# Kernel tuning notes

Measured on AMD Instinct MI355X. Metric: run time of the kernel, lower is better.

The kernel has to match this reference:

```python
import jax, jax.numpy as jnp
import numpy as np

VOXEL = 64          # voxel_size
MAX_DEPTH = 10.0    # depth_range[1]
SMIN, SMAX = -2.0, 2.0  # spatial_range


def setup_inputs() -> dict:
    key = jax.random.key(0)
    B, H, W = 32, 512, 512
    rgbd = jax.random.uniform(key, (B, 4, H, W), dtype=jnp.float32)
    # scale depth channel to a realistic metric range [0, 8) so that a
    # meaningful fraction of back-projected points falls inside [-2, 2]
    rgbd = rgbd.at[:, 3].multiply(8.0)
    return {"rgbd": rgbd}


def reference(rgbd):
    B, C, H, W = rgbd.shape
    V = VOXEL
    dt = rgbd.dtype

    rgb = jnp.transpose(rgbd[:, :3], (0, 2, 3, 1))   # [B,H,W,3]
    d = rgbd[:, 3]                                   # [B,H,W]

    # intrinsics is None -> default pinhole
    fx = fy = min(H, W) / 2.0
    cx, cy = W / 2.0, H / 2.0

    u = jnp.arange(W, dtype=dt)[None, None, :]       # column index (x)
    v = jnp.arange(H, dtype=dt)[None, :, None]       # row index (y)

    # depth -> pointcloud (per pixel)
    x = (u - cx) * d / fx
    y = (v - cy) * d / fy
    pts = jnp.stack([x, y, d], axis=-1)              # [B,H,W,3]

    depth_valid = (d > 0) & (d < MAX_DEPTH) & jnp.isfinite(d)

    # pointcloud -> voxel coordinates
    coords = jnp.round((pts - SMIN) / (SMAX - SMIN) * (V - 1)).astype(jnp.int32)
    in_range = jnp.all((coords >= 0) & (coords < V), axis=-1)
    mask = depth_valid & in_range                    # [B,H,W]
    coords = jnp.clip(coords, 0, V - 1)

    b_idx = jnp.arange(B, dtype=jnp.int32)[:, None, None]
    lin = ((b_idx * V + coords[..., 0]) * V + coords[..., 1]) * V + coords[..., 2]
    lin = lin.reshape(-1)                            # [B*H*W]
    w = mask.astype(dt).reshape(-1)                  # [B*H*W]

    nseg = B * V * V * V
    count = jax.ops.segment_sum(w, lin, num_segments=nseg)                 # [B*V^3]
    csum = jax.ops.segment_sum(rgb.reshape(-1, 3) * w[:, None], lin,
                               num_segments=nseg)                          # [B*V^3,3]

    occ = (count > 0).astype(dt)                                           # occupancy = 1 where any point lands
    color = jnp.where(count[:, None] > 0,
                      csum / jnp.maximum(count, 1.0)[:, None],
                      jnp.zeros((), dt))                                   # mean color per occupied voxel

    occ = occ.reshape(B, V, V, V)
    color = color.reshape(B, V, V, V, 3).transpose(0, 4, 1, 2, 3)
    return jnp.concatenate([occ[:, None], color], axis=1)  # [B,4,V,V,V]
```

## Files before the change

kernel.cpp:

```cpp
#include <hip/hip_runtime.h>
#include <math.h>


constexpr int V = 64;
constexpr int V3 = V * V * V;
constexpr int Wd = 512, Hd = 512;
constexpr int NPIX = Wd * Hd;
constexpr int NBUCKET = 32 * 64;
constexpr unsigned CAP = 30000;
constexpr float CQ = 32768.0f;
constexpr int PPB = 2048;
constexpr int CHUNKS = NPIX / PPB;

__device__ __forceinline__ bool unproject(int w, int h, float d,
                                          int& ix, int& iy, int& iz) {
    if (!(d > 0.0f) || !(d < 10.0f) || !isfinite(d)) return false;
    const float fx = 256.0f, cx = 256.0f, cy = 256.0f;
    float x = (((float)w - cx) * d) / fx;
    float y = (((float)h - cy) * d) / fx;
    float tx = rintf(((x + 2.0f) * 0.25f) * 63.0f);
    float ty = rintf(((y + 2.0f) * 0.25f) * 63.0f);
    float tz = rintf(((d + 2.0f) * 0.25f) * 63.0f);
    ix = (int)tx; iy = (int)ty; iz = (int)tz;
    return !(ix < 0 || ix >= V || iy < 0 || iy >= V ||
             iz < 0 || iz >= V);
}

__global__ void dtv_cursor_init(unsigned* __restrict__ cursor) {
    int i = blockIdx.x * blockDim.x + threadIdx.x;
    cursor[i] = (unsigned)i * CAP;
}

__global__ void __launch_bounds__(256)
dtv_append4(const float* __restrict__ rgbd,
            unsigned* __restrict__ cursor,
            unsigned long long* __restrict__ entries) {
    int blk = blockIdx.x;
    int b = blk >> 7, chunk = blk & (CHUNKS - 1), t = threadIdx.x;

    __shared__ unsigned lcnt[64];
    __shared__ unsigned lpre[64];
    __shared__ unsigned labs[64];
    __shared__ unsigned long long stage[PPB];
    __shared__ unsigned short bkt[PPB];

    if (t < 64) lcnt[t] = 0;
    __syncthreads();

    const float* bb = rgbd + (size_t)b * 4 * NPIX;
    const float4* r4 = (const float4*)(bb) + chunk * (PPB / 4);
    const float4* g4 = (const float4*)(bb + (size_t)NPIX) + chunk * (PPB / 4);
    const float4* b4 = (const float4*)(bb + (size_t)2 * NPIX) + chunk * (PPB / 4);
    const float4* d4 = (const float4*)(bb + (size_t)3 * NPIX) + chunk * (PPB / 4);
    int pbase = chunk * PPB;

    float4 dv[2], rv[2], gv[2], bv[2];
#pragma unroll
    for (int i = 0; i < 2; ++i) dv[i] = d4[t + i * 256];
#pragma unroll
    for (int i = 0; i < 2; ++i) {
        rv[i] = r4[t + i * 256];
        gv[i] = g4[t + i * 256];
        bv[i] = b4[t + i * 256];
    }

    unsigned meta[8];
#pragma unroll
    for (int i = 0; i < 2; ++i) {
        int p0 = pbase + 4 * (t + i * 256);
#pragma unroll
        for (int j = 0; j < 4; ++j) {
            float d = (j == 0) ? dv[i].x : (j == 1) ? dv[i].y
                    : (j == 2) ? dv[i].z : dv[i].w;
            int pix = p0 + j;
            int h = pix >> 9, w = pix & (Wd - 1);
            int ix, iy, iz;
            if (unproject(w, h, d, ix, iy, iz)) {
                unsigned off = atomicAdd(&lcnt[ix], 1u);
                meta[i * 4 + j] = ((unsigned)ix << 24) | ((unsigned)iy << 18) |
                                  ((unsigned)iz << 12) | off;
            } else {
                meta[i * 4 + j] = 0xFFFFFFFFu;
            }
        }
    }
    __syncthreads();

    if (t < 64) {
        unsigned c = lcnt[t];
        unsigned s = c;
#pragma unroll
        for (int off = 1; off < 64; off <<= 1) {
            unsigned v = __shfl_up(s, off, 64);
            if (t >= off) s += v;
        }
        lpre[t] = s - c;
        labs[t] = c ? atomicAdd(&cursor[b * 64 + t], c) : 0u;
    }
    __syncthreads();

#pragma unroll
    for (int i = 0; i < 2; ++i) {
#pragma unroll
        for (int j = 0; j < 4; ++j) {
            unsigned m = meta[i * 4 + j];
            if (m == 0xFFFFFFFFu) continue;
            unsigned ix = m >> 24, iy = (m >> 18) & 63u, iz = (m >> 12) & 63u;
            unsigned off = m & 0xFFFu;
            float r  = (j == 0) ? rv[i].x : (j == 1) ? rv[i].y
                     : (j == 2) ? rv[i].z : rv[i].w;
            float g  = (j == 0) ? gv[i].x : (j == 1) ? gv[i].y
                     : (j == 2) ? gv[i].z : gv[i].w;
            float bl = (j == 0) ? bv[i].x : (j == 1) ? bv[i].y
                     : (j == 2) ? bv[i].z : bv[i].w;
            unsigned long long r16 = (unsigned long long)(unsigned)rintf(r  * CQ);
            unsigned long long g16 = (unsigned long long)(unsigned)rintf(g  * CQ);
            unsigned long long b16 = (unsigned long long)(unsigned)rintf(bl * CQ);
            unsigned slot = lpre[ix] + off;
            stage[slot] = ((unsigned long long)iy << 54) |
                          ((unsigned long long)iz << 48) |
                          (r16 << 32) | (g16 << 16) | b16;
            bkt[slot] = (unsigned short)ix;
        }
    }
    __syncthreads();

    unsigned total = lpre[63] + lcnt[63];
    for (unsigned e = t; e < total; e += 256) {
        unsigned ix = bkt[e];
        unsigned pos = labs[ix] + (e - lpre[ix]);
        unsigned kk = (unsigned)(b * 64) + ix;
        if (pos < (kk + 1) * CAP)
            entries[(size_t)pos] = stage[e];
    }
}

__global__ void __launch_bounds__(256)
dtv_reduce4(const ulonglong2* __restrict__ entries2,
            const unsigned* __restrict__ cursor,
            float* __restrict__ out) {
    int bq = blockIdx.x;
    int kk = bq >> 2;
    unsigned quad = (unsigned)(bq & 3);
    int b = kk >> 6, ix = kk & 63, t = threadIdx.x;

    __shared__ unsigned long long ldsA[1024];
    __shared__ unsigned long long ldsB[1024];

    unsigned basew = (unsigned)kk * CAP;
    unsigned cnt = cursor[kk] - basew;
    if (cnt > CAP) cnt = CAP;
    unsigned npair = cnt >> 1;
    size_t base2 = (size_t)kk * (CAP / 2);

    ulonglong2 e2;
    if (t < (int)npair) e2 = entries2[base2 + t];

    ulonglong2* zA = (ulonglong2*)ldsA;
    ulonglong2* zB = (ulonglong2*)ldsB;
#pragma unroll
    for (int i = 0; i < 2; ++i) {
        zA[t + i * 256] = ulonglong2{0ULL, 0ULL};
        zB[t + i * 256] = ulonglong2{0ULL, 0ULL};
    }
    __syncthreads();

    auto accum = [&](unsigned long long p) {
        if (((unsigned)(p >> 58) & 3u) != quad) return;
        unsigned iy4 = (unsigned)(p >> 54) & 15u;
        unsigned iz  = (unsigned)(p >> 48) & 63u;
        unsigned v = iy4 * 64u + iz;
        atomicAdd(&ldsA[v], (1ULL << 32) | ((p >> 32) & 0xFFFFULL));
        atomicAdd(&ldsB[v], (((p >> 16) & 0xFFFFULL) << 32) | (p & 0xFFFFULL));
    };

    for (unsigned j = t; j < npair; j += 256) {
        ulonglong2 cur = e2;
        unsigned jn = j + 256;
        if (jn < npair) e2 = entries2[base2 + jn];
        accum(cur.x);
        accum(cur.y);
    }
    if ((cnt & 1u) && t == 0) {
        const unsigned long long* e1 = (const unsigned long long*)entries2;
        accum(e1[(size_t)basew + cnt - 1]);
    }
    __syncthreads();

    float* p0 = out + (size_t)b * 4 * V3 + (size_t)ix * 4096 + quad * 1024;
    int v0 = t * 4;
    float4 o0, o1, o2, o3;
#pragma unroll
    for (int j = 0; j < 4; ++j) {
        unsigned long long A = ldsA[v0 + j], Bw = ldsB[v0 + j];
        unsigned c = (unsigned)(A >> 32);
        float occ = 0.0f, r = 0.0f, g = 0.0f, bl = 0.0f;
        if (c) {
            float inv = 1.0f / (CQ * (float)c);
            occ = 1.0f;
            r  = (float)(unsigned)(A  & 0xFFFFFFFFULL) * inv;
            g  = (float)(unsigned)(Bw >> 32)            * inv;
            bl = (float)(unsigned)(Bw & 0xFFFFFFFFULL)  * inv;
        }
        (&o0.x)[j] = occ; (&o1.x)[j] = r; (&o2.x)[j] = g; (&o3.x)[j] = bl;
    }
    ((float4*)(p0))[t]                  = o0;
    ((float4*)(p0 + (size_t)V3))[t]     = o1;
    ((float4*)(p0 + (size_t)2 * V3))[t] = o2;
    ((float4*)(p0 + (size_t)3 * V3))[t] = o3;
}

__global__ void dtv_scatter_f32(const float* __restrict__ rgbd,
                                float* __restrict__ acc) {
    int idx = blockIdx.x * blockDim.x + threadIdx.x;
    int b   = idx >> 18;
    int pix = idx & (NPIX - 1);
    int h   = pix >> 9;
    int w   = pix & (Wd - 1);
    const float* base = rgbd + (size_t)b * 4 * NPIX;
    float d = base[(size_t)3 * NPIX + pix];
    int ix, iy, iz;
    if (!unproject(w, h, d, ix, iy, iz)) return;
    float r  = base[pix];
    float g  = base[(size_t)NPIX + pix];
    float bl = base[(size_t)2 * NPIX + pix];
    float* ob = acc + (size_t)b * 4 * V3;
    int vlin = (ix * V + iy) * V + iz;
    atomicAdd(ob + vlin, 1.0f);
    atomicAdd(ob + (size_t)V3 + vlin, r);
    atomicAdd(ob + (size_t)2 * V3 + vlin, g);
    atomicAdd(ob + (size_t)3 * V3 + vlin, bl);
}

__global__ void dtv_finalize_f32(float* __restrict__ out) {
    int idx = blockIdx.x * blockDim.x + threadIdx.x;
    int b    = idx >> 18;
    int vlin = idx & (V3 - 1);
    float* p = out + (size_t)b * 4 * V3;
    float c  = p[vlin];
    float r  = p[(size_t)V3 + vlin];
    float g  = p[(size_t)2 * V3 + vlin];
    float bl = p[(size_t)3 * V3 + vlin];
    bool occ = (c > 0.0f);
    p[vlin]                  = occ ? 1.0f : 0.0f;
    p[(size_t)V3 + vlin]     = occ ? (r / c)  : 0.0f;
    p[(size_t)2 * V3 + vlin] = occ ? (g / c)  : 0.0f;
    p[(size_t)3 * V3 + vlin] = occ ? (bl / c) : 0.0f;
}

extern "C" void kernel_launch(void* const* d_in, const int* in_sizes, int n_in,
                              void* d_out, int out_size, void* d_ws, size_t ws_size,
                              hipStream_t stream) {
    const float* rgbd = (const float*)d_in[0];
    float* out = (float*)d_out;
    const int B = in_sizes[0] / (4 * NPIX);

    size_t need = 8192 + (size_t)NBUCKET * CAP * sizeof(unsigned long long);

    if (B == 32 && ws_size >= need) {
        unsigned* cursor = (unsigned*)d_ws;
        unsigned long long* entries =
            (unsigned long long*)((char*)d_ws + 8192);
        dtv_cursor_init<<<NBUCKET / 256, 256, 0, stream>>>(cursor);
        dtv_append4    <<<B * CHUNKS, 256, 0, stream>>>(rgbd, cursor, entries);
        dtv_reduce4    <<<NBUCKET * 4, 256, 0, stream>>>((const ulonglong2*)entries,
                                                         cursor, out);
    } else {
        hipMemsetAsync(d_out, 0, (size_t)out_size * sizeof(float), stream);
        int total_pix = B * NPIX;
        int total_vox = B * V3;
        dtv_scatter_f32 <<<(total_pix + 255) / 256, 256, 0, stream>>>(rgbd, out);
        dtv_finalize_f32<<<(total_vox + 255) / 256, 256, 0, stream>>>(out);
    }
}
```

Measured before the change: 246.5 us.

## Pack bucket index into entry, use nontemporal IO, reorder reduce blocks by load

Color quantization drops to 14 bits so the x-bucket index fits in the 64-bit staged entry, which removes the separate shared-memory bucket array and its writes. Input loads and output stores become nontemporal to avoid cache pollution on streaming data. The reduce grid is remapped so blocks for central x buckets, which likely receive the most points, are scheduled first and the tail is better balanced. Lower color precision increases quantization error in the mean colors.

```diff
diff --git a/kernel.cpp b/kernel.cpp
--- a/kernel.cpp
+++ b/kernel.cpp
@@ -8,9 +8,11 @@
 constexpr int NPIX = Wd * Hd;
 constexpr int NBUCKET = 32 * 64;
 constexpr unsigned CAP = 30000;
-constexpr float CQ = 32768.0f;
+constexpr float CQ = 16384.0f;
 constexpr int PPB = 2048;
 constexpr int CHUNKS = NPIX / PPB;
+
+typedef float f4 __attribute__((ext_vector_type(4)));
 
 __device__ __forceinline__ bool unproject(int w, int h, float d,
                                           int& ix, int& iy, int& iz) {
@@ -42,26 +44,25 @@
     __shared__ unsigned lpre[64];
     __shared__ unsigned labs[64];
     __shared__ unsigned long long stage[PPB];
-    __shared__ unsigned short bkt[PPB];
 
     if (t < 64) lcnt[t] = 0;
     __syncthreads();
 
     const float* bb = rgbd + (size_t)b * 4 * NPIX;
-    const float4* r4 = (const float4*)(bb) + chunk * (PPB / 4);
-    const float4* g4 = (const float4*)(bb + (size_t)NPIX) + chunk * (PPB / 4);
-    const float4* b4 = (const float4*)(bb + (size_t)2 * NPIX) + chunk * (PPB / 4);
-    const float4* d4 = (const float4*)(bb + (size_t)3 * NPIX) + chunk * (PPB / 4);
+    const f4* r4 = (const f4*)(bb) + chunk * (PPB / 4);
+    const f4* g4 = (const f4*)(bb + (size_t)NPIX) + chunk * (PPB / 4);
+    const f4* b4 = (const f4*)(bb + (size_t)2 * NPIX) + chunk * (PPB / 4);
+    const f4* d4 = (const f4*)(bb + (size_t)3 * NPIX) + chunk * (PPB / 4);
     int pbase = chunk * PPB;
 
-    float4 dv[2], rv[2], gv[2], bv[2];
-#pragma unroll
-    for (int i = 0; i < 2; ++i) dv[i] = d4[t + i * 256];
-#pragma unroll
-    for (int i = 0; i < 2; ++i) {
-        rv[i] = r4[t + i * 256];
-        gv[i] = g4[t + i * 256];
-        bv[i] = b4[t + i * 256];
+    f4 dv[2], rv[2], gv[2], bv[2];
+#pragma unroll
+    for (int i = 0; i < 2; ++i) dv[i] = __builtin_nontemporal_load(&d4[t + i * 256]);
+#pragma unroll
+    for (int i = 0; i < 2; ++i) {
+        rv[i] = __builtin_nontemporal_load(&r4[t + i * 256]);
+        gv[i] = __builtin_nontemporal_load(&g4[t + i * 256]);
+        bv[i] = __builtin_nontemporal_load(&b4[t + i * 256]);
     }
 
     unsigned meta[8];
@@ -70,8 +71,7 @@
         int p0 = pbase + 4 * (t + i * 256);
 #pragma unroll
         for (int j = 0; j < 4; ++j) {
-            float d = (j == 0) ? dv[i].x : (j == 1) ? dv[i].y
-                    : (j == 2) ? dv[i].z : dv[i].w;
+            float d = dv[i][j];
             int pix = p0 + j;
             int h = pix >> 9, w = pix & (Wd - 1);
             int ix, iy, iz;
@@ -107,31 +107,29 @@
             if (m == 0xFFFFFFFFu) continue;
             unsigned ix = m >> 24, iy = (m >> 18) & 63u, iz = (m >> 12) & 63u;
             unsigned off = m & 0xFFFu;
-            float r  = (j == 0) ? rv[i].x : (j == 1) ? rv[i].y
-                     : (j == 2) ? rv[i].z : rv[i].w;
-            float g  = (j == 0) ? gv[i].x : (j == 1) ? gv[i].y
-                     : (j == 2) ? gv[i].z : gv[i].w;
-            float bl = (j == 0) ? bv[i].x : (j == 1) ? bv[i].y
-                     : (j == 2) ? bv[i].z : bv[i].w;
-            unsigned long long r16 = (unsigned long long)(unsigned)rintf(r  * CQ);
-            unsigned long long g16 = (unsigned long long)(unsigned)rintf(g  * CQ);
-            unsigned long long b16 = (unsigned long long)(unsigned)rintf(bl * CQ);
+            float r  = rv[i][j];
+            float g  = gv[i][j];
+            float bl = bv[i][j];
+            unsigned long long r14 = (unsigned long long)(unsigned)rintf(r  * CQ);
+            unsigned long long g14 = (unsigned long long)(unsigned)rintf(g  * CQ);
+            unsigned long long b14 = (unsigned long long)(unsigned)rintf(bl * CQ);
             unsigned slot = lpre[ix] + off;
-            stage[slot] = ((unsigned long long)iy << 54) |
-                          ((unsigned long long)iz << 48) |
-                          (r16 << 32) | (g16 << 16) | b16;
-            bkt[slot] = (unsigned short)ix;
+            stage[slot] = ((unsigned long long)ix << 57) |
+                          ((unsigned long long)iy << 51) |
+                          ((unsigned long long)iz << 45) |
+                          (r14 << 30) | (g14 << 15) | b14;
         }
     }
     __syncthreads();
 
     unsigned total = lpre[63] + lcnt[63];
     for (unsigned e = t; e < total; e += 256) {
-        unsigned ix = bkt[e];
+        unsigned long long ent = stage[e];
+        unsigned ix = (unsigned)(ent >> 57) & 63u;
         unsigned pos = labs[ix] + (e - lpre[ix]);
         unsigned kk = (unsigned)(b * 64) + ix;
         if (pos < (kk + 1) * CAP)
-            entries[(size_t)pos] = stage[e];
+            entries[(size_t)pos] = ent;
     }
 }
 
@@ -140,9 +138,12 @@
             const unsigned* __restrict__ cursor,
             float* __restrict__ out) {
     int bq = blockIdx.x;
-    int kk = bq >> 2;
+    unsigned rank = (unsigned)bq >> 7;
+    int ix = (rank & 1u) ? (31 - (int)(rank >> 1)) : (32 + (int)(rank >> 1));
+    int b  = (bq >> 2) & 31;
     unsigned quad = (unsigned)(bq & 3);
-    int b = kk >> 6, ix = kk & 63, t = threadIdx.x;
+    int kk = b * 64 + ix;
+    int t = threadIdx.x;
 
     __shared__ unsigned long long ldsA[1024];
     __shared__ unsigned long long ldsB[1024];
@@ -166,12 +167,12 @@
     __syncthreads();
 
     auto accum = [&](unsigned long long p) {
-        if (((unsigned)(p >> 58) & 3u) != quad) return;
-        unsigned iy4 = (unsigned)(p >> 54) & 15u;
-        unsigned iz  = (unsigned)(p >> 48) & 63u;
+        if (((unsigned)(p >> 55) & 3u) != quad) return;
+        unsigned iy4 = (unsigned)(p >> 51) & 15u;
+        unsigned iz  = (unsigned)(p >> 45) & 63u;
         unsigned v = iy4 * 64u + iz;
-        atomicAdd(&ldsA[v], (1ULL << 32) | ((p >> 32) & 0xFFFFULL));
-        atomicAdd(&ldsB[v], (((p >> 16) & 0xFFFFULL) << 32) | (p & 0xFFFFULL));
+        atomicAdd(&ldsA[v], (1ULL << 32) | ((p >> 30) & 0x7FFFULL));
+        atomicAdd(&ldsB[v], (((p >> 15) & 0x7FFFULL) << 32) | (p & 0x7FFFULL));
     };
 
     for (unsigned j = t; j < npair; j += 256) {
@@ -189,7 +190,7 @@
 
     float* p0 = out + (size_t)b * 4 * V3 + (size_t)ix * 4096 + quad * 1024;
     int v0 = t * 4;
-    float4 o0, o1, o2, o3;
+    f4 o0, o1, o2, o3;
 #pragma unroll
     for (int j = 0; j < 4; ++j) {
         unsigned long long A = ldsA[v0 + j], Bw = ldsB[v0 + j];
@@ -202,12 +203,12 @@
             g  = (float)(unsigned)(Bw >> 32)            * inv;
             bl = (float)(unsigned)(Bw & 0xFFFFFFFFULL)  * inv;
         }
-        (&o0.x)[j] = occ; (&o1.x)[j] = r; (&o2.x)[j] = g; (&o3.x)[j] = bl;
-    }
-    ((float4*)(p0))[t]                  = o0;
-    ((float4*)(p0 + (size_t)V3))[t]     = o1;
-    ((float4*)(p0 + (size_t)2 * V3))[t] = o2;
-    ((float4*)(p0 + (size_t)3 * V3))[t] = o3;
+        o0[j] = occ; o1[j] = r; o2[j] = g; o3[j] = bl;
+    }
+    __builtin_nontemporal_store(o0, (f4*)(p0) + t);
+    __builtin_nontemporal_store(o1, (f4*)(p0 + (size_t)V3) + t);
+    __builtin_nontemporal_store(o2, (f4*)(p0 + (size_t)2 * V3) + t);
+    __builtin_nontemporal_store(o3, (f4*)(p0 + (size_t)3 * V3) + t);
 }
 
 __global__ void dtv_scatter_f32(const float* __restrict__ rgbd,
@@ -266,7 +267,7 @@
         dtv_reduce4    <<<NBUCKET * 4, 256, 0, stream>>>((const ulonglong2*)entries,
                                                          cursor, out);
     } else {
-        hipMemsetAsync(d_out, 0, (size_t)out_size * sizeof(float), stream);
+        (void)hipMemsetAsync(d_out, 0, (size_t)out_size * sizeof(float), stream);
         int total_pix = B * NPIX;
         int total_vox = B * V3;
         dtv_scatter_f32 <<<(total_pix + 255) / 256, 256, 0, stream>>>(rgbd, out);
```

Measured after the change: 242.2 us. About the same (-1.7%).
